# Kernel tuning notes

Measured on AMD Instinct MI355X. Metric: run time of the kernel, lower is better.

## Reference

```python
import jax, jax.numpy as jnp
import numpy as np

TEMP = 0.07


def setup_inputs() -> dict:
    key = jax.random.key(0)
    kq, kk = jax.random.split(key)
    B, D = 8192, 128
    q = jax.random.normal(kq, (B, D), dtype=jnp.float32)
    k = jax.random.normal(kk, (B, D), dtype=jnp.float32)
    return {"q": q, "k": k}


def reference(q, k):
    # features = cat([q, k], dim=0); F.normalize(dim=1)
    B = q.shape[0]
    N = 2 * B
    f = jnp.concatenate([q, k], axis=0)
    f = f / jnp.maximum(jnp.linalg.norm(f, axis=1, keepdims=True), 1e-12)
    sim = f @ f.T  # [N, N]

    i = jnp.arange(N)
    p = (i + B) % N                      # index of the positive pair of row i
    pos = sim[i, p][:, None]             # [N, 1]

    # negatives: all columns except the diagonal (i) and the positive (p),
    # in original column order (matches boolean-mask ordering in torch).
    a = jnp.minimum(i, p)[:, None]       # [N, 1]
    b = jnp.maximum(i, p)[:, None]
    j = jnp.arange(N - 2)[None, :]       # [1, N-2]
    c = j + (j >= a)                     # skip first excluded column
    c = c + (c >= b)                     # skip second excluded column
    neg = jnp.take_along_axis(sim, c, axis=1)  # [N, N-2]

    logits = jnp.concatenate([pos, neg], axis=1) / TEMP  # [N, N-1]
    labels = jnp.zeros((N,), dtype=jnp.int32)
    return logits, labels
```

## Files before the change

kernel.cpp:

```cpp
#include <hip/hip_runtime.h>
#include <hip/hip_bf16.h>
#include <stdint.h>

#define B_ROWS 8192
#define N_TOT  16384
#define D_DIM  128
#define SCALE_SQRT_INVT 3.7796447300922722f

typedef __bf16 bf16x8 __attribute__((ext_vector_type(8)));
typedef float  f32x4  __attribute__((ext_vector_type(4)));

__global__ void simclr_norm_kernel(const float* __restrict__ q,
                                   const float* __restrict__ k,
                                   unsigned int* __restrict__ fb) {
    const int lane = threadIdx.x & 63;
    const int row  = blockIdx.x * 4 + (threadIdx.x >> 6);
    const float* src = (row < B_ROWS) ? (q + (size_t)row * D_DIM)
                                      : (k + (size_t)(row - B_ROWS) * D_DIM);
    float2 v = ((const float2*)src)[lane];
    float s = v.x * v.x + v.y * v.y;
#pragma unroll
    for (int off = 32; off > 0; off >>= 1) s += __shfl_xor(s, off);
    float rn = SCALE_SQRT_INVT / fmaxf(sqrtf(s), 1e-12f);
    union { __bf16 h[2]; unsigned int u; } pk;
    pk.h[0] = (__bf16)(v.x * rn);
    pk.h[1] = (__bf16)(v.y * rn);
    fb[(size_t)row * 64 + lane] = pk.u;
}

__global__ __launch_bounds__(256, 2) void simclr_gemm_kernel(
        const unsigned short* __restrict__ fb, float* __restrict__ out) {
    __shared__ char lds[32768];

    const int bid = blockIdx.x;
    const int r0  = (bid >> 1) * 64;
    const int h   = bid & 1;
    const int lane = threadIdx.x & 63;
    const int w    = threadIdx.x >> 6;
    const int rl = lane & 15;
    const int kg = lane >> 4;

    const char* fbb = (const char*)fb;
    const int cbase = h * 8192;
    const int base_s = (h == 0) ? 1 : 0;

    bf16x8 afr[4][4];
#pragma unroll
    for (int m = 0; m < 4; ++m)
#pragma unroll
        for (int ks = 0; ks < 4; ++ks)
            afr[m][ks] = *(const bf16x8*)(fbb + (size_t)(r0 + m * 16 + rl) * 256 + ks * 64 + kg * 16);

    bf16x8 bcur[4][2], bnxt[4][2];
#pragma unroll
    for (int ks = 0; ks < 4; ++ks)
#pragma unroll
        for (int n = 0; n < 2; ++n)
            bcur[ks][n] = *(const bf16x8*)(fbb + (size_t)(cbase + w * 32 + n * 16 + rl) * 256 + ks * 64 + kg * 16);

    for (int t = 0; t < 64; ++t) {
        const int c0 = cbase + t * 128;

        if (t < 63) {
#pragma unroll
            for (int ks = 0; ks < 4; ++ks)
#pragma unroll
                for (int n = 0; n < 2; ++n)
                    bnxt[ks][n] = *(const bf16x8*)(fbb + (size_t)(c0 + 128 + w * 32 + n * 16 + rl) * 256 + ks * 64 + kg * 16);
        }
        __builtin_amdgcn_sched_barrier(0);

        f32x4 acc[4][2];
#pragma unroll
        for (int m = 0; m < 4; ++m)
#pragma unroll
            for (int n = 0; n < 2; ++n) acc[m][n] = (f32x4){0.f, 0.f, 0.f, 0.f};
#pragma unroll
        for (int ks = 0; ks < 4; ++ks)
#pragma unroll
            for (int m = 0; m < 4; ++m)
#pragma unroll
                for (int n = 0; n < 2; ++n)
                    acc[m][n] = __builtin_amdgcn_mfma_f32_16x16x32_bf16(bcur[ks][n], afr[m][ks], acc[m][n], 0, 0, 0);

#pragma unroll
        for (int m = 0; m < 4; ++m) {
            const int row = m * 16 + rl;
#pragma unroll
            for (int n = 0; n < 2; ++n) {
                const int colb = w * 128 + n * 64 + kg * 16;
                *(f32x4*)(lds + row * 512 + (colb ^ ((row & 7) << 4))) = acc[m][n];
            }
        }
        asm volatile("s_waitcnt lgkmcnt(0)" ::: "memory");
        __builtin_amdgcn_sched_barrier(0);
        __builtin_amdgcn_s_barrier();
        __builtin_amdgcn_sched_barrier(0);

#pragma unroll
        for (int j = 0; j < 8; ++j) {
            const int row = w * 16 + j * 2 + (lane >> 5);
            const int i   = r0 + row;
            const int ch  = lane & 31;
            f32x4 v = *(const f32x4*)(lds + row * 512 + ((ch * 16) ^ ((row & 7) << 4)));
            const int sc = cbase + (i & (B_ROWS - 1));
            float* orow = out + (size_t)i * (N_TOT - 1);
            const unsigned rel = (unsigned)(sc - c0);
            if (__builtin_expect(rel < 128u, 0)) {
                const bool isdiag = ((i >> 13) == h);
#pragma unroll
                for (int e = 0; e < 4; ++e) {
                    const int c = c0 + ch * 4 + e;
                    const float val = v[e];
                    if (c == sc) { if (!isdiag) orow[0] = val; }
                    else orow[c + base_s - (c > sc)] = val;
                }
            } else {
                const int s = base_s - (c0 > sc ? 1 : 0);
                __builtin_memcpy(orow + c0 + s + ch * 4, &v, sizeof(v));
            }
        }
        __builtin_amdgcn_sched_barrier(0);
        __builtin_amdgcn_s_barrier();
        __builtin_amdgcn_sched_barrier(0);

        if (t < 63) {
#pragma unroll
            for (int ks = 0; ks < 4; ++ks)
#pragma unroll
                for (int n = 0; n < 2; ++n)
                    bcur[ks][n] = bnxt[ks][n];
        }
    }
}

__global__ void simclr_zero_labels(float* __restrict__ out) {
    out[(size_t)N_TOT * (N_TOT - 1) + blockIdx.x * 256 + threadIdx.x] = 0.0f;
}

extern "C" void kernel_launch(void* const* d_in, const int* in_sizes, int n_in,
                              void* d_out, int out_size, void* d_ws, size_t ws_size,
                              hipStream_t stream) {
    const float* q = (const float*)d_in[0];
    const float* k = (const float*)d_in[1];
    float* out = (float*)d_out;
    unsigned int* fb = (unsigned int*)d_ws;

    simclr_norm_kernel<<<N_TOT / 4, 256, 0, stream>>>(q, k, fb);
    simclr_zero_labels<<<N_TOT / 256, 256, 0, stream>>>(out);
    simclr_gemm_kernel<<<512, 256, 0, stream>>>((const unsigned short*)d_ws, out);
}
```

Baseline: 362.3 us.

## Batch four column tiles in LDS before storing, one block per row strip

Each block now covers the full 16384 columns for its 64 rows (256 blocks instead of 512). It accumulates four 128-column MFMA tiles into a 128 KB dynamic LDS buffer before writing out, so each wave writes full 1 KB row segments per store pass and halves the barrier count. The aim is longer, more coalesced global writes of the large logits output and less synchronisation. The cost is fewer blocks (only 256, so some CUs may sit idle), occupancy of one block per CU, and a large LDS footprint.

```diff
diff --git a/kernel.cpp b/kernel.cpp
--- a/kernel.cpp
+++ b/kernel.cpp
@@ -28,21 +28,17 @@
     fb[(size_t)row * 64 + lane] = pk.u;
 }
 
-__global__ __launch_bounds__(256, 2) void simclr_gemm_kernel(
+__global__ __launch_bounds__(256, 1) void simclr_gemm_kernel(
         const unsigned short* __restrict__ fb, float* __restrict__ out) {
-    __shared__ char lds[32768];
+    extern __shared__ char lds[];
 
     const int bid = blockIdx.x;
-    const int r0  = (bid >> 1) * 64;
-    const int h   = bid & 1;
+    const int r0  = bid * 64;
     const int lane = threadIdx.x & 63;
     const int w    = threadIdx.x >> 6;
     const int rl = lane & 15;
     const int kg = lane >> 4;
-
     const char* fbb = (const char*)fb;
-    const int cbase = h * 8192;
-    const int base_s = (h == 0) ? 1 : 0;
 
     bf16x8 afr[4][4];
 #pragma unroll
@@ -56,12 +52,12 @@
     for (int ks = 0; ks < 4; ++ks)
 #pragma unroll
         for (int n = 0; n < 2; ++n)
-            bcur[ks][n] = *(const bf16x8*)(fbb + (size_t)(cbase + w * 32 + n * 16 + rl) * 256 + ks * 64 + kg * 16);
+            bcur[ks][n] = *(const bf16x8*)(fbb + (size_t)(w * 32 + n * 16 + rl) * 256 + ks * 64 + kg * 16);
 
-    for (int t = 0; t < 64; ++t) {
-        const int c0 = cbase + t * 128;
+    for (int t = 0; t < 128; ++t) {
+        const int c0 = t * 128;
 
-        if (t < 63) {
+        if (t < 127) {
 #pragma unroll
             for (int ks = 0; ks < 4; ++ks)
 #pragma unroll
@@ -83,48 +79,59 @@
                 for (int n = 0; n < 2; ++n)
                     acc[m][n] = __builtin_amdgcn_mfma_f32_16x16x32_bf16(bcur[ks][n], afr[m][ks], acc[m][n], 0, 0, 0);
 
+        const int sub = t & 3;
 #pragma unroll
         for (int m = 0; m < 4; ++m) {
             const int row = m * 16 + rl;
 #pragma unroll
             for (int n = 0; n < 2; ++n) {
-                const int colb = w * 128 + n * 64 + kg * 16;
-                *(f32x4*)(lds + row * 512 + (colb ^ ((row & 7) << 4))) = acc[m][n];
+                const int colb = sub * 512 + w * 128 + n * 64 + kg * 16;
+                *(f32x4*)(lds + row * 2048 + (colb ^ ((row & 7) << 4))) = acc[m][n];
             }
         }
-        asm volatile("s_waitcnt lgkmcnt(0)" ::: "memory");
-        __builtin_amdgcn_sched_barrier(0);
-        __builtin_amdgcn_s_barrier();
-        __builtin_amdgcn_sched_barrier(0);
 
+        if (sub == 3) {
+            asm volatile("s_waitcnt lgkmcnt(0)" ::: "memory");
+            __builtin_amdgcn_sched_barrier(0);
+            __builtin_amdgcn_s_barrier();
+            __builtin_amdgcn_sched_barrier(0);
+
+            const int c0s = (t >> 2) * 512;
 #pragma unroll
-        for (int j = 0; j < 8; ++j) {
-            const int row = w * 16 + j * 2 + (lane >> 5);
-            const int i   = r0 + row;
-            const int ch  = lane & 31;
-            f32x4 v = *(const f32x4*)(lds + row * 512 + ((ch * 16) ^ ((row & 7) << 4)));
-            const int sc = cbase + (i & (B_ROWS - 1));
-            float* orow = out + (size_t)i * (N_TOT - 1);
-            const unsigned rel = (unsigned)(sc - c0);
-            if (__builtin_expect(rel < 128u, 0)) {
-                const bool isdiag = ((i >> 13) == h);
+            for (int j = 0; j < 16; ++j) {
+                const int row = w * 16 + j;
+                const int i   = r0 + row;
+                const int p   = i ^ B_ROWS;
+                const int a   = i & (B_ROWS - 1);
+                const int b   = a | B_ROWS;
+                float* orow = out + (size_t)i * (N_TOT - 1);
 #pragma unroll
-                for (int e = 0; e < 4; ++e) {
-                    const int c = c0 + ch * 4 + e;
-                    const float val = v[e];
-                    if (c == sc) { if (!isdiag) orow[0] = val; }
-                    else orow[c + base_s - (c > sc)] = val;
+                for (int hh = 0; hh < 2; ++hh) {
+                    const int cq = c0s + hh * 256;
+                    f32x4 v = *(const f32x4*)(lds + row * 2048 +
+                                ((hh * 1024 + lane * 16) ^ ((row & 7) << 4)));
+                    if (__builtin_expect((unsigned)(a - cq) < 256u ||
+                                         (unsigned)(b - cq) < 256u, 0)) {
+#pragma unroll
+                        for (int e = 0; e < 4; ++e) {
+                            const int c = cq + lane * 4 + e;
+                            const float val = v[e];
+                            if (c == i) continue;
+                            if (c == p) { orow[0] = val; continue; }
+                            orow[c + 1 - (c > a) - (c > b)] = val;
+                        }
+                    } else {
+                        const int s = 1 - (a < cq) - (b < cq);
+                        __builtin_memcpy(orow + cq + s + lane * 4, &v, sizeof(v));
+                    }
                 }
-            } else {
-                const int s = base_s - (c0 > sc ? 1 : 0);
-                __builtin_memcpy(orow + c0 + s + ch * 4, &v, sizeof(v));
             }
+            __builtin_amdgcn_sched_barrier(0);
+            __builtin_amdgcn_s_barrier();
+            __builtin_amdgcn_sched_barrier(0);
         }
-        __builtin_amdgcn_sched_barrier(0);
-        __builtin_amdgcn_s_barrier();
-        __builtin_amdgcn_sched_barrier(0);
 
-        if (t < 63) {
+        if (t < 127) {
 #pragma unroll
             for (int ks = 0; ks < 4; ++ks)
 #pragma unroll
@@ -146,7 +153,10 @@
     float* out = (float*)d_out;
     unsigned int* fb = (unsigned int*)d_ws;
 
+    hipFuncSetAttribute((const void*)simclr_gemm_kernel,
+                        hipFuncAttributeMaxDynamicSharedMemorySize, 131072);
+
     simclr_norm_kernel<<<N_TOT / 4, 256, 0, stream>>>(q, k, fb);
     simclr_zero_labels<<<N_TOT / 256, 256, 0, stream>>>(out);
-    simclr_gemm_kernel<<<512, 256, 0, stream>>>((const unsigned short*)d_ws, out);
+    simclr_gemm_kernel<<<256, 256, 131072, stream>>>((const unsigned short*)d_ws, out);
 }
```

Measured after the change: 395.4 us. +9.1%, slower.
